# Kernel tuning notes

Measured on AMD Instinct MI355X. Metric: run time of the kernel, lower is better.

## Reference

```python
import jax, jax.numpy as jnp
import numpy as np
from jax import lax

VOCAB, EMBED, HIDDEN, TAGS, SEQ = 50000, 300, 512, 12, 4096
START, STOP = 10, 11
NEG = -10000.0


def setup_inputs() -> dict:
    key = jax.random.key(0)
    ks = jax.random.split(key, 10)
    p = lambda k, shape: (jax.random.normal(k, shape, jnp.float32) * 0.1)
    transitions = jnp.zeros((TAGS, TAGS), jnp.float32)
    transitions = transitions.at[START, :].set(NEG).at[:, STOP].set(NEG)
    return {
        "sentence": jax.random.randint(ks[0], (SEQ,), 0, VOCAB),
        "embed_table": p(ks[1], (VOCAB, EMBED)),
        "Wih_f": p(ks[2], (4 * HIDDEN, EMBED)),
        "Whh_f": p(ks[3], (4 * HIDDEN, HIDDEN)),
        "bih_f": jnp.zeros((4 * HIDDEN,), jnp.float32),
        "bhh_f": jnp.zeros((4 * HIDDEN,), jnp.float32),
        "Wih_b": p(ks[4], (4 * HIDDEN, EMBED)),
        "Whh_b": p(ks[5], (4 * HIDDEN, HIDDEN)),
        "bih_b": jnp.zeros((4 * HIDDEN,), jnp.float32),
        "bhh_b": jnp.zeros((4 * HIDDEN,), jnp.float32),
        "W_out": p(ks[6], (TAGS, 2 * HIDDEN)),
        "b_out": jnp.zeros((TAGS,), jnp.float32),
        "transitions": transitions,
    }


def run_lstm(x, Wih, Whh, bih, bhh, reverse=False):
    # x: [T, E]; PyTorch gate order i, f, g, o
    H = Whh.shape[1]
    xg = x @ Wih.T + (bih + bhh)  # [T, 4H] precompute input projection

    def step(carry, g_in):
        h, c = carry
        g = g_in + h @ Whh.T
        i, f, gg, o = jnp.split(g, 4)
        i, f, o = jax.nn.sigmoid(i), jax.nn.sigmoid(f), jax.nn.sigmoid(o)
        c = f * c + i * jnp.tanh(gg)
        h = o * jnp.tanh(c)
        return (h, c), h

    init = (jnp.zeros((H,), x.dtype), jnp.zeros((H,), x.dtype))
    _, hs = lax.scan(step, init, xg, reverse=reverse)
    return hs  # [T, H], time-ordered


def lstm_features(sentence, embed_table, Wih_f, Whh_f, bih_f, bhh_f,
                  Wih_b, Whh_b, bih_b, bhh_b, W_out, b_out):
    emb = embed_table[sentence]  # [T, E]
    h_f = run_lstm(emb, Wih_f, Whh_f, bih_f, bhh_f, reverse=False)
    h_b = run_lstm(emb, Wih_b, Whh_b, bih_b, bhh_b, reverse=True)
    h = jnp.concatenate([h_f, h_b], axis=-1)  # [T, 2H]
    # dropout is identity in eval mode
    return h @ W_out.T + b_out  # [T, TAGS]


def viterbi(feats, transitions):
    K = feats.shape[1]
    init = jnp.full((K,), NEG, feats.dtype).at[START].set(0.0)

    def step(fv, feat):
        ntv = fv[None, :] + transitions  # [next, prev]
        bp = jnp.argmax(ntv, axis=1)
        return jnp.max(ntv, axis=1) + feat, bp

    fv, bps = lax.scan(step, init, feats)  # bps: [T, K]
    term = fv + transitions[STOP]
    term = term.at[STOP].set(NEG).at[START].set(NEG)
    best = jnp.argmax(term)
    score = term[best]

    def back(tag, bp):
        prev = bp[tag]
        return prev, prev

    _, chain = lax.scan(back, best, bps, reverse=True)  # chain[t] = tag at t-1
    path = jnp.concatenate([chain[1:], best[None]])  # [T] best tag sequence
    return score, path


def reference(sentence, embed_table, Wih_f, Whh_f, bih_f, bhh_f,
              Wih_b, Whh_b, bih_b, bhh_b, W_out, b_out, transitions):
    feats = lstm_features(sentence, embed_table, Wih_f, Whh_f, bih_f, bhh_f,
                          Wih_b, Whh_b, bih_b, bhh_b, W_out, b_out)
    score, path = viterbi(feats, transitions)
    return score, path
```

## Files before the change

### kernel.cpp

```cpp
#include <hip/hip_runtime.h>
#include <hip/hip_bf16.h>
#include <stdint.h>

#define SEQ_T 4096
#define EMB   300
#define HID   512
#define G4    2048
#define NTAG  12
#define TAG_START 10
#define TAG_STOP  11
#define NEGV  -10000.0f
#define NCHUNK 256
#define CLEN   16

#define OFF_XG    0
#define OFF_H     (OFF_XG + 2 * SEQ_T * G4)
#define OFF_HS    (OFF_H + 4096)
#define OFF_FEATS (OFF_HS + 2 * SEQ_T * HID)
#define OFF_VM    (OFF_FEATS + SEQ_T * NTAG)
#define OFF_VB    (OFF_VM + NCHUNK * 144)
#define OFF_VSC   (OFF_VB + NCHUNK * NTAG)
#define OFF_VP    (OFF_VSC + 8)
#define OFF_VMAP  (OFF_VP + NCHUNK * NTAG * 2)
#define WS_FLOATS (OFF_VMAP + NCHUNK * 2)

__device__ __forceinline__ float sigm_(float x) {
    return __fdividef(1.f, 1.f + __expf(-x));
}
__device__ __forceinline__ float tanh_(float x) {
    x = fminf(fmaxf(x, -15.f), 15.f);
    float e = __expf(2.f * x);
    return __fdividef(e - 1.f, e + 1.f);
}

#define POLL4(Q0, Q1, Q2, Q3, PREV, SRC, OUT) do {                          \
    int idx_;                                                               \
    asm volatile(                                                           \
        "global_load_dwordx2 %[q0], %[a], off sc0 sc1\n\t"                 \
        "global_load_dwordx2 %[q1], %[a], off sc0 sc1\n\t"                 \
        "global_load_dwordx2 %[q2], %[a], off sc0 sc1\n\t"                 \
        "global_load_dwordx2 %[q3], %[a], off sc0 sc1\n\t"                 \
        "1:\n\t"                                                            \
        "s_waitcnt vmcnt(3)\n\t"                                            \
        "v_cmp_eq_u64 vcc, %[q0], %[pv]\n\t"                                \
        "s_cbranch_vccz 2f\n\t"                                             \
        "global_load_dwordx2 %[q0], %[a], off sc0 sc1\n\t"                 \
        "s_waitcnt vmcnt(3)\n\t"                                            \
        "v_cmp_eq_u64 vcc, %[q1], %[pv]\n\t"                                \
        "s_cbranch_vccz 3f\n\t"                                             \
        "global_load_dwordx2 %[q1], %[a], off sc0 sc1\n\t"                 \
        "s_waitcnt vmcnt(3)\n\t"                                            \
        "v_cmp_eq_u64 vcc, %[q2], %[pv]\n\t"                                \
        "s_cbranch_vccz 4f\n\t"                                             \
        "global_load_dwordx2 %[q2], %[a], off sc0 sc1\n\t"                 \
        "s_waitcnt vmcnt(3)\n\t"                                            \
        "v_cmp_eq_u64 vcc, %[q3], %[pv]\n\t"                                \
        "s_cbranch_vccz 5f\n\t"                                             \
        "global_load_dwordx2 %[q3], %[a], off sc0 sc1\n\t"                 \
        "s_branch 1b\n\t"                                                   \
        "2:\n\t"                                                            \
        "s_mov_b32 %[i], 0\n\t"                                             \
        "s_branch 6f\n\t"                                                   \
        "3:\n\t"                                                            \
        "s_mov_b32 %[i], 1\n\t"                                             \
        "s_branch 6f\n\t"                                                   \
        "4:\n\t"                                                            \
        "s_mov_b32 %[i], 2\n\t"                                             \
        "s_branch 6f\n\t"                                                   \
        "5:\n\t"                                                            \
        "s_mov_b32 %[i], 3\n\t"                                             \
        "6:\n\t"                                                            \
        : [q0] "+v"(Q0), [q1] "+v"(Q1), [q2] "+v"(Q2), [q3] "+v"(Q3),      \
          [i] "=s"(idx_)                                                    \
        : [a] "v"(SRC), [pv] "v"(PREV)                                      \
        : "vcc", "memory");                                                 \
    OUT = (idx_ == 0) ? Q0 : (idx_ == 1) ? Q1 : (idx_ == 2) ? Q2 : Q3;     \
    PREV = OUT;                                                             \
} while (0)

__global__ __launch_bounds__(256) void k_xg(const int* __restrict__ sent,
                                            const float* __restrict__ table,
                                            const float* __restrict__ Wih_f,
                                            const float* __restrict__ bih_f,
                                            const float* __restrict__ bhh_f,
                                            const float* __restrict__ Wih_b,
                                            const float* __restrict__ bih_b,
                                            const float* __restrict__ bhh_b,
                                            float* __restrict__ ws) {
    __shared__ float As[64 * 105];
    __shared__ float Bs[64 * 105];
    __shared__ int rows[64];
    const int dir = blockIdx.z;
    const int g0  = blockIdx.x << 6;
    const int t0  = blockIdx.y << 6;
    const int tid = threadIdx.x;
    const float* __restrict__ Wih = dir ? Wih_b : Wih_f;
    const float* __restrict__ bih = dir ? bih_b : bih_f;
    const float* __restrict__ bhh = dir ? bhh_b : bhh_f;
    if (tid < 64) rows[tid] = sent[t0 + tid];
    if (blockIdx.x == 0 && blockIdx.y == 0) {
        for (int e = tid; e < 2048; e += 256)
            ws[OFF_H + (size_t)blockIdx.z * 2048 + e] = 0.f;
    }
    __syncthreads();

    const int tg = (tid & 15) << 2;
    const int tp = (tid >> 4) << 2;
    float acc[4][4] = {{0.f}};

    for (int c = 0; c < 3; ++c) {
        const int k0 = c * 100;
        for (int e = tid; e < 64 * 100; e += 256) {
            int ti = e / 100, kk = e - ti * 100;
            As[ti * 105 + kk] = table[(size_t)rows[ti] * EMB + k0 + kk];
        }
        for (int e = tid; e < 64 * 100; e += 256) {
            int gi = e / 100, kk = e - gi * 100;
            Bs[gi * 105 + kk] = Wih[(size_t)(g0 + gi) * EMB + k0 + kk];
        }
        __syncthreads();
        for (int kk = 0; kk < 100; ++kk) {
            float a0 = As[(tp + 0) * 105 + kk];
            float a1 = As[(tp + 1) * 105 + kk];
            float a2 = As[(tp + 2) * 105 + kk];
            float a3 = As[(tp + 3) * 105 + kk];
            float b0 = Bs[(tg + 0) * 105 + kk];
            float b1 = Bs[(tg + 1) * 105 + kk];
            float b2 = Bs[(tg + 2) * 105 + kk];
            float b3 = Bs[(tg + 3) * 105 + kk];
            acc[0][0] = fmaf(a0, b0, acc[0][0]); acc[0][1] = fmaf(a0, b1, acc[0][1]);
            acc[0][2] = fmaf(a0, b2, acc[0][2]); acc[0][3] = fmaf(a0, b3, acc[0][3]);
            acc[1][0] = fmaf(a1, b0, acc[1][0]); acc[1][1] = fmaf(a1, b1, acc[1][1]);
            acc[1][2] = fmaf(a1, b2, acc[1][2]); acc[1][3] = fmaf(a1, b3, acc[1][3]);
            acc[2][0] = fmaf(a2, b0, acc[2][0]); acc[2][1] = fmaf(a2, b1, acc[2][1]);
            acc[2][2] = fmaf(a2, b2, acc[2][2]); acc[2][3] = fmaf(a2, b3, acc[2][3]);
            acc[3][0] = fmaf(a3, b0, acc[3][0]); acc[3][1] = fmaf(a3, b1, acc[3][1]);
            acc[3][2] = fmaf(a3, b2, acc[3][2]); acc[3][3] = fmaf(a3, b3, acc[3][3]);
        }
        __syncthreads();
    }
    float4 bv4 = *(const float4*)(bih + g0 + tg);
    float4 bh4 = *(const float4*)(bhh + g0 + tg);
    float4 bb = make_float4(bv4.x + bh4.x, bv4.y + bh4.y, bv4.z + bh4.z, bv4.w + bh4.w);
    #pragma unroll
    for (int i = 0; i < 4; ++i) {
        float4 r = make_float4(acc[i][0] + bb.x, acc[i][1] + bb.y,
                               acc[i][2] + bb.z, acc[i][3] + bb.w);
        *(float4*)(ws + OFF_XG + ((size_t)dir * SEQ_T + t0 + tp + i) * G4 + g0 + tg) = r;
    }
}

__global__ __launch_bounds__(512, 2) void k_scan(const float* __restrict__ Whh_f,
                                                 const float* __restrict__ Whh_b,
                                                 float* __restrict__ ws) {
    __shared__ float h_sh[2][8 * 68];
    const int bid = blockIdx.x;
    const int dir = bid >> 5;
    const int wg  = bid & 31;
    const int tid = threadIdx.x;
    const int wave = tid >> 6;
    const int lane = tid & 63;
    const int s  = lane >> 4;
    const int qq = (lane >> 3) & 1;
    const int p  = lane & 7;
    const int hu   = (wg << 4) + (wave << 1) + qq;
    const int gate = (s << 9) + hu;
    const float* __restrict__ Whh = dir ? Whh_b : Whh_f;

    float* xg = ws + OFF_XG + (size_t)dir * SEQ_T * G4;
    unsigned long long* hbuf = (unsigned long long*)(ws + OFF_H);
    float* hs = ws + OFF_HS + (size_t)dir * SEQ_T * HID;

    float4 w[16];
    {
        const float4* wrow = (const float4*)(Whh + (size_t)gate * HID + (p << 6));
        #pragma unroll
        for (int j = 0; j < 16; ++j) w[j] = wrow[j];
    }

    const bool owner = (s == 0) && (p == 0);
    float c = 0.f;
    float xg_cur = 0.f;
    if (p == 0) xg_cur = xg[(size_t)(dir ? (SEQ_T - 1) : 0) * G4 + gate];

    unsigned long long pa0 = 0, pa1 = 0, pa2 = 0, pa3 = 0;
    unsigned long long pb0 = 0, pb1 = 0, pb2 = 0, pb3 = 0;
    unsigned long long prevA = 0, prevB = 0;

    for (int k = 0; k < SEQ_T; ++k) {
        const int time = dir ? (SEQ_T - 1 - k) : k;
        float xg_nxt = 0.f;
        if (p == 0 && (k + 1) < SEQ_T)
            xg_nxt = xg[(size_t)(dir ? (time - 1) : (time + 1)) * G4 + gate];

        float acc = xg_cur;
        if (k > 0) {
            const int par = (k - 1) & 1;
            unsigned long long* src = hbuf + ((size_t)(par << 1) + dir) * HID + tid;
            unsigned long long v;
            if (par == 0) {
                POLL4(pa0, pa1, pa2, pa3, prevA, src, v);
            } else {
                POLL4(pb0, pb1, pb2, pb3, prevB, src, v);
            }
            h_sh[par][wave * 68 + lane] = __uint_as_float((unsigned)v);
            __syncthreads();
            const float4* hp = (const float4*)(&h_sh[par][p * 68]);
            float ax = 0.f, ay = 0.f, az = 0.f, aw = 0.f;
            #pragma unroll
            for (int j = 0; j < 16; ++j) {
                float4 hv = hp[j];
                ax = fmaf(w[j].x, hv.x, ax);
                ay = fmaf(w[j].y, hv.y, ay);
                az = fmaf(w[j].z, hv.z, az);
                aw = fmaf(w[j].w, hv.w, aw);
            }
            acc += (ax + ay) + (az + aw);
        }
        acc += __shfl_xor(acc, 1);
        acc += __shfl_xor(acc, 2);
        acc += __shfl_xor(acc, 4);
        const int base = lane & 15;
        float gi = __shfl(acc, base + 0);
        float gf = __shfl(acc, base + 16);
        float gg = __shfl(acc, base + 32);
        float go = __shfl(acc, base + 48);
        if (owner) {
            float iv = sigm_(gi), fv = sigm_(gf), gv = tanh_(gg), ov = sigm_(go);
            c = fmaf(fv, c, iv * gv);
            float h = ov * tanh_(c);
            unsigned long long pv = ((unsigned long long)(unsigned)(k + 1) << 32) |
                                    (unsigned long long)__float_as_uint(h);
            __hip_atomic_store(&hbuf[((size_t)((k & 1) << 1) + dir) * HID + hu], pv,
                               __ATOMIC_RELAXED, __HIP_MEMORY_SCOPE_AGENT);
            hs[(size_t)time * HID + hu] = h;
        }
        xg_cur = xg_nxt;
    }
    asm volatile("s_waitcnt vmcnt(0)" ::: "memory");
}

__global__ __launch_bounds__(256) void k_feats(const float* __restrict__ Wout,
                                               const float* __restrict__ bout,
                                               float* __restrict__ ws) {
    const int t = blockIdx.x;
    const int tid = threadIdx.x;
    const float* hsf = ws + OFF_HS;
    const float* hsb = ws + OFF_HS + (size_t)SEQ_T * HID;
    float4 h4 = (tid < 128) ? ((const float4*)(hsf + (size_t)t * HID))[tid]
                            : ((const float4*)(hsb + (size_t)t * HID))[tid - 128];
    float pj[NTAG];
    #pragma unroll
    for (int j = 0; j < NTAG; ++j) {
        float4 wv = ((const float4*)(Wout + (size_t)j * 2 * HID))[tid];
        pj[j] = h4.x * wv.x + h4.y * wv.y + h4.z * wv.z + h4.w * wv.w;
    }
    #pragma unroll
    for (int j = 0; j < NTAG; ++j) {
        #pragma unroll
        for (int m = 1; m < 64; m <<= 1) pj[j] += __shfl_xor(pj[j], m);
    }
    __shared__ float red[4][NTAG];
    if ((tid & 63) == 0) {
        #pragma unroll
        for (int j = 0; j < NTAG; ++j) red[tid >> 6][j] = pj[j];
    }
    __syncthreads();
    if (tid < NTAG) {
        float v = red[0][tid] + red[1][tid] + red[2][tid] + red[3][tid] + bout[tid];
        ws[OFF_FEATS + (size_t)t * NTAG + tid] = v;
    }
}

__global__ __launch_bounds__(192) void k_vitA(const float* __restrict__ trans,
                                              float* __restrict__ ws) {
    __shared__ float M[NTAG][13];
    __shared__ float T[NTAG][NTAG];
    const int c = blockIdx.x;
    const int tid = threadIdx.x;
    const float* feats = ws + OFF_FEATS;
    const int j = tid / NTAG, i = tid - j * NTAG;
    if (tid < 144) T[j][i] = trans[tid];
    __syncthreads();
    float cur = 0.f;
    const int t0 = c * CLEN;
    if (tid < 144) cur = T[j][i] + feats[(size_t)t0 * NTAG + j];
    for (int t = t0 + 1; t < t0 + CLEN; ++t) {
        if (tid < 144) M[j][i] = cur;
        __syncthreads();
        if (tid < 144) {
            float fj = feats[(size_t)t * NTAG + j];
            float best = -3.4e38f;
            #pragma unroll
            for (int kk = 0; kk < NTAG; ++kk)
                best = fmaxf(best, T[j][kk] + M[kk][i]);
            cur = best + fj;
        }
        __syncthreads();
    }
    if (tid < 144) ws[OFF_VM + (size_t)c * 144 + tid] = cur;
}

__global__ __launch_bounds__(192) void k_vitB(const float* __restrict__ trans,
                                              float* __restrict__ ws,
                                              float* __restrict__ out) {
    __shared__ float Ms[NTAG][13];
    __shared__ float fvs[NTAG];
    const int tid = threadIdx.x;
    const int j = tid / NTAG, i = tid - j * NTAG;
    if (tid < NTAG) fvs[tid] = (tid == TAG_START) ? 0.f : NEGV;
    float m = (tid < 144) ? ws[OFF_VM + tid] : 0.f;
    for (int c = 0; c < NCHUNK; ++c) {
        if (tid < 144) Ms[j][i] = m;
        __syncthreads();
        if (tid < 144 && (c + 1) < NCHUNK)
            m = ws[OFF_VM + (size_t)(c + 1) * 144 + tid];
        float nf = 0.f;
        if (tid < NTAG) {
            ws[OFF_VB + (size_t)c * NTAG + tid] = fvs[tid];
            float best = -3.4e38f;
            #pragma unroll
            for (int kk = 0; kk < NTAG; ++kk)
                best = fmaxf(best, Ms[tid][kk] + fvs[kk]);
            nf = best;
        }
        __syncthreads();
        if (tid < NTAG) fvs[tid] = nf;
        __syncthreads();
    }
    if (tid == 0) {
        float bsc = -3.4e38f; int btag = 0;
        for (int q = 0; q < NTAG; ++q) {
            float tv = fvs[q] + trans[TAG_STOP * NTAG + q];
            if (q == TAG_START || q == TAG_STOP) tv = NEGV;
            if (tv > bsc) { bsc = tv; btag = q; }
        }
        out[0] = bsc;
        ((int*)(ws + OFF_VSC))[0] = btag;
    }
}

__global__ __launch_bounds__(256) void k_vitC(const float* __restrict__ trans,
                                              float* __restrict__ ws) {
    const int lane = threadIdx.x & 63;
    const int c = blockIdx.x * 4 + (threadIdx.x >> 6);
    const float* feats = ws + OFF_FEATS;
    float Trow[NTAG];
    #pragma unroll
    for (int i = 0; i < NTAG; ++i)
        Trow[i] = (lane < NTAG) ? trans[lane * NTAG + i] : -1e30f;
    float fv = (lane < NTAG) ? ws[OFF_VB + (size_t)c * NTAG + lane] : NEGV;

    unsigned bpLo[CLEN], bpHi[CLEN];
    const int t0 = c * CLEN;
    #pragma unroll
    for (int tt = 0; tt < CLEN; ++tt) {
        const int t = t0 + tt;
        float vv[NTAG];
        #pragma unroll
        for (int i = 0; i < NTAG; ++i) vv[i] = __shfl(fv, i) + Trow[i];
        float m0; int i0;
        {
            float a0 = vv[0];  int b0 = 0;  if (vv[1]  > a0) { a0 = vv[1];  b0 = 1; }
            float a1 = vv[2];  int b1 = 2;  if (vv[3]  > a1) { a1 = vv[3];  b1 = 3; }
            float a2 = vv[4];  int b2 = 4;  if (vv[5]  > a2) { a2 = vv[5];  b2 = 5; }
            float a3 = vv[6];  int b3 = 6;  if (vv[7]  > a3) { a3 = vv[7];  b3 = 7; }
            float a4 = vv[8];  int b4 = 8;  if (vv[9]  > a4) { a4 = vv[9];  b4 = 9; }
            float a5 = vv[10]; int b5 = 10; if (vv[11] > a5) { a5 = vv[11]; b5 = 11; }
            if (a1 > a0) { a0 = a1; b0 = b1; }
            if (a3 > a2) { a2 = a3; b2 = b3; }
            if (a5 > a4) { a4 = a5; b4 = b5; }
            if (a2 > a0) { a0 = a2; b0 = b2; }
            if (a4 > a0) { a0 = a4; b0 = b4; }
            m0 = a0; i0 = b0;
        }
        fv = (lane < NTAG) ? (m0 + feats[(size_t)t * NTAG + lane]) : NEGV;
        unsigned nib = (lane < NTAG) ? ((unsigned)i0 << ((lane & 7) << 2)) : 0u;
        nib |= __shfl_xor(nib, 1);
        nib |= __shfl_xor(nib, 2);
        nib |= __shfl_xor(nib, 4);
        bpLo[tt] = __shfl(nib, 0);
        bpHi[tt] = __shfl(nib, 8);
    }
    if (lane < NTAG) {
        int tag = lane;
        unsigned long long pk = 0ull;
        #pragma unroll
        for (int tt = CLEN - 1; tt >= 0; --tt) {
            pk |= ((unsigned long long)(unsigned)tag) << (tt << 2);
            unsigned wsel = (tag < 8) ? bpLo[tt] : bpHi[tt];
            tag = (int)((wsel >> ((tag & 7) << 2)) & 15u);
        }
        ((unsigned long long*)(ws + OFF_VP))[(size_t)c * NTAG + lane] = pk;
        unsigned long long mc = ((unsigned long long)(unsigned)tag) << (lane << 2);
        mc |= __shfl_xor(mc, 1);
        mc |= __shfl_xor(mc, 2);
        mc |= __shfl_xor(mc, 4);
        mc |= __shfl_xor(mc, 8);
        if (lane == 0) ((unsigned long long*)(ws + OFF_VMAP))[c] = mc;
    }
}

__global__ __launch_bounds__(64) void k_vitD(float* __restrict__ ws,
                                             float* __restrict__ out) {
    const int lane = threadIdx.x;
    const unsigned long long* vp = (const unsigned long long*)(ws + OFF_VP);
    const unsigned long long* vmap = (const unsigned long long*)(ws + OFF_VMAP);
    int tag = ((const int*)(ws + OFF_VSC))[0];
    for (int c = NCHUNK - 1; c >= 0; --c) {
        unsigned long long row = (lane < NTAG) ? vp[(size_t)c * NTAG + lane] : 0ull;
        unsigned long long mp = vmap[c];
        unsigned long long pk = __shfl(row, tag);
        if (lane < CLEN)
            out[c * CLEN + lane + 1] = (float)((pk >> (lane << 2)) & 15ull);
        tag = (int)((mp >> (tag << 2)) & 15ull);
    }
}

extern "C" void kernel_launch(void* const* d_in, const int* in_sizes, int n_in,
                              void* d_out, int out_size, void* d_ws, size_t ws_size,
                              hipStream_t stream) {
    const int*   sent  = (const int*)d_in[0];
    const float* table = (const float*)d_in[1];
    const float* Wih_f = (const float*)d_in[2];
    const float* Whh_f = (const float*)d_in[3];
    const float* bih_f = (const float*)d_in[4];
    const float* bhh_f = (const float*)d_in[5];
    const float* Wih_b = (const float*)d_in[6];
    const float* Whh_b = (const float*)d_in[7];
    const float* bih_b = (const float*)d_in[8];
    const float* bhh_b = (const float*)d_in[9];
    const float* Wout  = (const float*)d_in[10];
    const float* bout  = (const float*)d_in[11];
    const float* trans = (const float*)d_in[12];
    float* out = (float*)d_out;
    float* ws  = (float*)d_ws;
    if (ws_size < (size_t)WS_FLOATS * sizeof(float)) return;

    hipLaunchKernelGGL(k_xg, dim3(32, 64, 2), dim3(256), 0, stream, sent, table,
                       Wih_f, bih_f, bhh_f, Wih_b, bih_b, bhh_b, ws);
    hipLaunchKernelGGL(k_scan, dim3(64), dim3(512), 0, stream, Whh_f, Whh_b, ws);
    hipLaunchKernelGGL(k_feats, dim3(SEQ_T), dim3(256), 0, stream, Wout, bout, ws);
    hipLaunchKernelGGL(k_vitA, dim3(NCHUNK), dim3(192), 0, stream, trans, ws);
    hipLaunchKernelGGL(k_vitB, dim3(1), dim3(192), 0, stream, trans, ws, out);
    hipLaunchKernelGGL(k_vitC, dim3(NCHUNK / 4), dim3(256), 0, stream, trans, ws);
    hipLaunchKernelGGL(k_vitD, dim3(1), dim3(64), 0, stream, ws, out);
}
```

Baseline: 7.700 ms.

## Replicate h exchange buffer four ways and poll replicas with tag compare

The producer now writes each step's hidden-state value to four replica slots spaced apart in the workspace. Consumers poll the four replicas in rotation, with small sleeps between the initial loads. Readiness is checked by comparing the step tag in the upper 32 bits instead of inequality with the previous value. The goal is to spread the polling traffic across separate cache lines or channels so the cross-block handoff has less latency on the serial LSTM path. The cost is four times the store traffic per step, a larger workspace region, and a new wait condition whose correctness relies on each replica holding the exact step tag.

```diff
diff --git a/kernel.cpp b/kernel.cpp
--- a/kernel.cpp
+++ b/kernel.cpp
@@ -15,7 +15,7 @@
 
 #define OFF_XG    0
 #define OFF_H     (OFF_XG + 2 * SEQ_T * G4)
-#define OFF_HS    (OFF_H + 4096)
+#define OFF_HS    (OFF_H + 16384)
 #define OFF_FEATS (OFF_HS + 2 * SEQ_T * HID)
 #define OFF_VM    (OFF_FEATS + SEQ_T * NTAG)
 #define OFF_VB    (OFF_VM + NCHUNK * 144)
@@ -24,6 +24,8 @@
 #define OFF_VMAP  (OFF_VP + NCHUNK * NTAG * 2)
 #define WS_FLOATS (OFF_VMAP + NCHUNK * 2)
 
+#define REP_STRIDE 2048
+
 __device__ __forceinline__ float sigm_(float x) {
     return __fdividef(1.f, 1.f + __expf(-x));
 }
@@ -33,30 +35,41 @@
     return __fdividef(e - 1.f, e + 1.f);
 }
 
-#define POLL4(Q0, Q1, Q2, Q3, PREV, SRC, OUT) do {                          \
+#define POLL4T(Q0, Q1, Q2, Q3, T64, A0, A1, A2, A3, K64, OUT) do {          \
     int idx_;                                                               \
     asm volatile(                                                           \
-        "global_load_dwordx2 %[q0], %[a], off sc0 sc1\n\t"                 \
-        "global_load_dwordx2 %[q1], %[a], off sc0 sc1\n\t"                 \
-        "global_load_dwordx2 %[q2], %[a], off sc0 sc1\n\t"                 \
-        "global_load_dwordx2 %[q3], %[a], off sc0 sc1\n\t"                 \
+        "global_load_dwordx2 %[q0], %[a0], off sc0 sc1\n\t"                 \
+        "s_sleep 4\n\t"                                                     \
+        "global_load_dwordx2 %[q1], %[a1], off sc0 sc1\n\t"                 \
+        "s_sleep 4\n\t"                                                     \
+        "global_load_dwordx2 %[q2], %[a2], off sc0 sc1\n\t"                 \
+        "s_sleep 4\n\t"                                                     \
+        "global_load_dwordx2 %[q3], %[a3], off sc0 sc1\n\t"                 \
         "1:\n\t"                                                            \
         "s_waitcnt vmcnt(3)\n\t"                                            \
-        "v_cmp_eq_u64 vcc, %[q0], %[pv]\n\t"                                \
-        "s_cbranch_vccz 2f\n\t"                                             \
-        "global_load_dwordx2 %[q0], %[a], off sc0 sc1\n\t"                 \
+        "v_lshrrev_b64 %[t], 32, %[q0]\n\t"                                 \
+        "v_cmp_eq_u64 vcc, %[t], %[kk]\n\t"                                 \
+        "s_cmp_eq_u64 vcc, -1\n\t"                                          \
+        "s_cbranch_scc1 2f\n\t"                                             \
+        "global_load_dwordx2 %[q0], %[a0], off sc0 sc1\n\t"                 \
         "s_waitcnt vmcnt(3)\n\t"                                            \
-        "v_cmp_eq_u64 vcc, %[q1], %[pv]\n\t"                                \
-        "s_cbranch_vccz 3f\n\t"                                             \
-        "global_load_dwordx2 %[q1], %[a], off sc0 sc1\n\t"                 \
+        "v_lshrrev_b64 %[t], 32, %[q1]\n\t"                                 \
+        "v_cmp_eq_u64 vcc, %[t], %[kk]\n\t"                                 \
+        "s_cmp_eq_u64 vcc, -1\n\t"                                          \
+        "s_cbranch_scc1 3f\n\t"                                             \
+        "global_load_dwordx2 %[q1], %[a1], off sc0 sc1\n\t"                 \
         "s_waitcnt vmcnt(3)\n\t"                                            \
-        "v_cmp_eq_u64 vcc, %[q2], %[pv]\n\t"                                \
-        "s_cbranch_vccz 4f\n\t"                                             \
-        "global_load_dwordx2 %[q2], %[a], off sc0 sc1\n\t"                 \
+        "v_lshrrev_b64 %[t], 32, %[q2]\n\t"                                 \
+        "v_cmp_eq_u64 vcc, %[t], %[kk]\n\t"                                 \
+        "s_cmp_eq_u64 vcc, -1\n\t"                                          \
+        "s_cbranch_scc1 4f\n\t"                                             \
+        "global_load_dwordx2 %[q2], %[a2], off sc0 sc1\n\t"                 \
         "s_waitcnt vmcnt(3)\n\t"                                            \
-        "v_cmp_eq_u64 vcc, %[q3], %[pv]\n\t"                                \
-        "s_cbranch_vccz 5f\n\t"                                             \
-        "global_load_dwordx2 %[q3], %[a], off sc0 sc1\n\t"                 \
+        "v_lshrrev_b64 %[t], 32, %[q3]\n\t"                                 \
+        "v_cmp_eq_u64 vcc, %[t], %[kk]\n\t"                                 \
+        "s_cmp_eq_u64 vcc, -1\n\t"                                          \
+        "s_cbranch_scc1 5f\n\t"                                             \
+        "global_load_dwordx2 %[q3], %[a3], off sc0 sc1\n\t"                 \
         "s_branch 1b\n\t"                                                   \
         "2:\n\t"                                                            \
         "s_mov_b32 %[i], 0\n\t"                                             \
@@ -71,11 +84,11 @@
         "s_mov_b32 %[i], 3\n\t"                                             \
         "6:\n\t"                                                            \
         : [q0] "+v"(Q0), [q1] "+v"(Q1), [q2] "+v"(Q2), [q3] "+v"(Q3),      \
-          [i] "=s"(idx_)                                                    \
-        : [a] "v"(SRC), [pv] "v"(PREV)                                      \
+          [t] "=&v"(T64), [i] "=s"(idx_)                                    \
+        : [a0] "v"(A0), [a1] "v"(A1), [a2] "v"(A2), [a3] "v"(A3),          \
+          [kk] "v"(K64)                                                     \
         : "vcc", "memory");                                                 \
     OUT = (idx_ == 0) ? Q0 : (idx_ == 1) ? Q1 : (idx_ == 2) ? Q2 : Q3;     \
-    PREV = OUT;                                                             \
 } while (0)
 
 __global__ __launch_bounds__(256) void k_xg(const int* __restrict__ sent,
@@ -99,8 +112,8 @@
     const float* __restrict__ bhh = dir ? bhh_b : bhh_f;
     if (tid < 64) rows[tid] = sent[t0 + tid];
     if (blockIdx.x == 0 && blockIdx.y == 0) {
-        for (int e = tid; e < 2048; e += 256)
-            ws[OFF_H + (size_t)blockIdx.z * 2048 + e] = 0.f;
+        for (int e = tid; e < 8192; e += 256)
+            ws[OFF_H + (size_t)blockIdx.z * 8192 + e] = 0.f;
     }
     __syncthreads();
 
@@ -183,9 +196,10 @@
     float xg_cur = 0.f;
     if (p == 0) xg_cur = xg[(size_t)(dir ? (SEQ_T - 1) : 0) * G4 + gate];
 
-    unsigned long long pa0 = 0, pa1 = 0, pa2 = 0, pa3 = 0;
-    unsigned long long pb0 = 0, pb1 = 0, pb2 = 0, pb3 = 0;
-    unsigned long long prevA = 0, prevB = 0;
+    unsigned long long* cA0 = hbuf + (size_t)(0 * 2 + dir) * HID + tid;
+    unsigned long long* cB0 = hbuf + (size_t)(1 * 2 + dir) * HID + tid;
+
+    unsigned long long q0 = 0, q1 = 0, q2 = 0, q3 = 0, t64;
 
     for (int k = 0; k < SEQ_T; ++k) {
         const int time = dir ? (SEQ_T - 1 - k) : k;
@@ -196,13 +210,12 @@
         float acc = xg_cur;
         if (k > 0) {
             const int par = (k - 1) & 1;
-            unsigned long long* src = hbuf + ((size_t)(par << 1) + dir) * HID + tid;
+            const unsigned long long want = (unsigned long long)(unsigned)k;
+            unsigned long long* b0 = (par == 0) ? cA0 : cB0;
             unsigned long long v;
-            if (par == 0) {
-                POLL4(pa0, pa1, pa2, pa3, prevA, src, v);
-            } else {
-                POLL4(pb0, pb1, pb2, pb3, prevB, src, v);
-            }
+            POLL4T(q0, q1, q2, q3, t64,
+                   b0, b0 + REP_STRIDE, b0 + 2 * REP_STRIDE,
+                   b0 + 3 * REP_STRIDE, want, v);
             h_sh[par][wave * 68 + lane] = __uint_as_float((unsigned)v);
             __syncthreads();
             const float4* hp = (const float4*)(&h_sh[par][p * 68]);
@@ -231,8 +244,15 @@
             float h = ov * tanh_(c);
             unsigned long long pv = ((unsigned long long)(unsigned)(k + 1) << 32) |
                                     (unsigned long long)__float_as_uint(h);
-            __hip_atomic_store(&hbuf[((size_t)((k & 1) << 1) + dir) * HID + hu], pv,
-                               __ATOMIC_RELAXED, __HIP_MEMORY_SCOPE_AGENT);
+            unsigned long long* dst =
+                &hbuf[((size_t)((k & 1) << 1) + dir) * HID + hu];
+            __hip_atomic_store(dst, pv, __ATOMIC_RELAXED, __HIP_MEMORY_SCOPE_AGENT);
+            __hip_atomic_store(dst + REP_STRIDE, pv, __ATOMIC_RELAXED,
+                               __HIP_MEMORY_SCOPE_AGENT);
+            __hip_atomic_store(dst + 2 * REP_STRIDE, pv, __ATOMIC_RELAXED,
+                               __HIP_MEMORY_SCOPE_AGENT);
+            __hip_atomic_store(dst + 3 * REP_STRIDE, pv, __ATOMIC_RELAXED,
+                               __HIP_MEMORY_SCOPE_AGENT);
             hs[(size_t)time * HID + hu] = h;
         }
         xg_cur = xg_nxt;
```

Result: slower. 9.193 ms (+19.4%).
